# Optimization experiments

Hardware: AMD Instinct MI355X
Metric: run time of the kernel (lower is better)

## Reference

```python
import jax, jax.numpy as jnp
import numpy as np


def setup_inputs() -> dict:
    key = jax.random.key(0)
    kq, kk, kv = jax.random.split(key, 3)
    B, H, S, D = 1, 16, 4096, 64
    Q = jax.random.normal(kq, (B, H, S, D), dtype=jnp.float32)
    K = jax.random.normal(kk, (B, H, S, D), dtype=jnp.float32)
    V = jax.random.normal(kv, (B, H, S, D), dtype=jnp.float32)
    return {"Q": Q, "K": K, "V": V}


def reference(Q, K, V):
    # scores: [B, H, len_q, len_k], scaled by sqrt(dim_k)
    dim_k = K.shape[-1]
    scale = 1.0 / jnp.sqrt(jnp.asarray(dim_k, dtype=Q.dtype))
    scores = jnp.einsum("bhqd,bhkd->bhqk", Q, K) * scale
    attention = jax.nn.softmax(scores, axis=-1)
    context = jnp.einsum("bhqk,bhkd->bhqd", attention, V)
    return context
```

## Files before the change

kernel.cpp:

```cpp
#include <hip/hip_runtime.h>
#include <hip/hip_bf16.h>

typedef short bf16x8 __attribute__((ext_vector_type(8)));
typedef __bf16 bfv8  __attribute__((ext_vector_type(8)));
typedef __bf16 bfv4  __attribute__((ext_vector_type(4)));
typedef float f32x4  __attribute__((ext_vector_type(4)));

#define S_LEN 4096
#define DDIM  64
#define KVB   32
#define QBLK  128
#define NHEAD 16
#define THR   7.0f
#define VOFFB 4096
#define BUFSZ 9216

#define MFMA(a, b, c) __builtin_amdgcn_mfma_f32_16x16x32_bf16((a), (b), (c), 0, 0, 0)

static __device__ __forceinline__ float exp2v(float x) {
    return __builtin_amdgcn_exp2f(x);
}

static __device__ __forceinline__ int4 cvt8(float4 a, float4 b) {
    bfv8 r;
    r[0] = (__bf16)a.x; r[1] = (__bf16)a.y; r[2] = (__bf16)a.z; r[3] = (__bf16)a.w;
    r[4] = (__bf16)b.x; r[5] = (__bf16)b.y; r[6] = (__bf16)b.z; r[7] = (__bf16)b.w;
    return __builtin_bit_cast(int4, r);
}
static __device__ __forceinline__ int2 cvt4(f32x4 a) {
    bfv4 r;
    r[0] = (__bf16)a[0]; r[1] = (__bf16)a[1]; r[2] = (__bf16)a[2]; r[3] = (__bf16)a[3];
    return __builtin_bit_cast(int2, r);
}

static __device__ __forceinline__ bf16x8 ldfrag(const unsigned char* base, int row, int doff) {
    int addr = (row * 128 + doff * 2) ^ ((row & 7) << 4);
    return *reinterpret_cast<const bf16x8*>(base + addr);
}

static __device__ __forceinline__ void stage(unsigned char* base, int kdst, int vdst,
                                             int4 kv, int4 vv) {
    *reinterpret_cast<int4*>(base + kdst)         = kv;
    *reinterpret_cast<int4*>(base + VOFFB + vdst) = vv;
}

static __device__ __forceinline__ bf16x8 softmax_pb(f32x4 s0, f32x4 s1, float& m,
                                                    f32x4 acc[4], f32x4& lacc) {
    float mx = fmaxf(fmaxf(fmaxf(s0[0], s0[1]), s0[2]),
                     fmaxf(fmaxf(s0[3], s1[0]),
                           fmaxf(s1[1], fmaxf(s1[2], s1[3]))));
    if (!__all(mx <= m + THR)) {
        float pm = fmaxf(mx, __shfl_xor(mx, 16));
        pm = fmaxf(pm, __shfl_xor(pm, 32));
        float mn = fmaxf(m, pm);
        float al = exp2v(m - mn);
        #pragma unroll
        for (int dk = 0; dk < 4; ++dk)
            #pragma unroll
            for (int j = 0; j < 4; ++j) acc[dk][j] *= al;
        #pragma unroll
        for (int j = 0; j < 4; ++j) lacc[j] *= al;
        m = mn;
    }
    bfv8 r;
    #pragma unroll
    for (int j = 0; j < 4; ++j) {
        r[2 * j]     = (__bf16)exp2v(s0[j] - m);
        r[2 * j + 1] = (__bf16)exp2v(s1[j] - m);
    }
    return __builtin_bit_cast(bf16x8, r);
}

__global__ __launch_bounds__(256) void prep(
    const float* __restrict__ Kg, const float* __restrict__ Vg,
    unsigned short* __restrict__ wsKT, unsigned short* __restrict__ wsVT)
{
    const int h  = blockIdx.y;
    const int kt = blockIdx.x;
    const int t  = threadIdx.x;
    const int srow = t >> 3;
    const int sd   = (t & 7) * 8;
    const size_t src = (((size_t)h * S_LEN) + (size_t)kt * 32 + srow) * DDIM + sd;

    {
        float4 a = *reinterpret_cast<const float4*>(Kg + src);
        float4 b = *reinterpret_cast<const float4*>(Kg + src + 4);
        const int swK = (srow * 128 + sd * 2) ^ ((srow & 7) << 4);
        *reinterpret_cast<int4*>(reinterpret_cast<char*>(wsKT)
            + ((size_t)(h * 128 + kt) << 12) + swK) = cvt8(a, b);
    }

    __shared__ __align__(16) unsigned short vt[32][68];
    {
        float4 a = *reinterpret_cast<const float4*>(Vg + src);
        float4 b = *reinterpret_cast<const float4*>(Vg + src + 4);
        int4 w = cvt8(a, b);
        int2 lo = {w.x, w.y}, hi = {w.z, w.w};
        *reinterpret_cast<int2*>(&vt[srow][sd])     = lo;
        *reinterpret_cast<int2*>(&vt[srow][sd + 4]) = hi;
    }
    __syncthreads();
    {
        const int d  = t >> 2;
        const int p0 = (t & 3) * 8;
        unsigned short out[8];
        #pragma unroll
        for (int i = 0; i < 8; ++i) {
            int p   = p0 + i;
            int key = 4 * (p >> 3) + ((p & 7) >> 1) + 16 * (p & 1);
            out[i] = vt[key][d];
        }
        *reinterpret_cast<int4*>(wsVT + ((size_t)(h * 128 + kt) * 2048) + d * 32 + p0)
            = *reinterpret_cast<const int4*>(out);
    }
}

template <int KSPLIT>
__global__ __launch_bounds__(256, 4) void attn_fwd(
    const float* __restrict__ Qg, const unsigned short* __restrict__ wsKT,
    const unsigned short* __restrict__ wsVT, float* __restrict__ Og,
    unsigned short* __restrict__ wsO, float* __restrict__ wsML)
{
    const int nwg  = 32 * NHEAD * KSPLIT;
    const int f    = blockIdx.x;
    const int work = (f & 7) * (nwg >> 3) + (f >> 3);
    const int qb   = work & 31;
    const int h    = (work >> 5) & (NHEAD - 1);
    const int ks   = (KSPLIT > 1) ? (work >> 9) : 0;
    const int kt0  = ks * (128 / KSPLIT);
    const int NT   = 128 / KSPLIT;
    const int tid  = threadIdx.x;
    const int lane = tid & 63;
    const int wv   = tid >> 6;
    const int g    = lane >> 4;
    const int r16  = lane & 15;

    __shared__ __align__(16) unsigned char lds[2 * BUFSZ];

    const float QSC = 0.125f * 1.44269504088896f;
    const int qrow0 = qb * QBLK + wv * 32 + r16;
    bf16x8 qf0[2], qf1[2];
    {
        const float* qp0 = Qg + ((size_t)h * S_LEN + qrow0) * DDIM;
        const float* qp1 = qp0 + 16 * DDIM;
        #pragma unroll
        for (int c = 0; c < 2; ++c) {
            float4 x = *reinterpret_cast<const float4*>(qp0 + 32 * c + 8 * g);
            float4 y = *reinterpret_cast<const float4*>(qp0 + 32 * c + 8 * g + 4);
            float4 xs = {x.x * QSC, x.y * QSC, x.z * QSC, x.w * QSC};
            float4 ys = {y.x * QSC, y.y * QSC, y.z * QSC, y.w * QSC};
            qf0[c] = __builtin_bit_cast(bf16x8, cvt8(xs, ys));
            x = *reinterpret_cast<const float4*>(qp1 + 32 * c + 8 * g);
            y = *reinterpret_cast<const float4*>(qp1 + 32 * c + 8 * g + 4);
            xs = {x.x * QSC, x.y * QSC, x.z * QSC, x.w * QSC};
            ys = {y.x * QSC, y.y * QSC, y.z * QSC, y.w * QSC};
            qf1[c] = __builtin_bit_cast(bf16x8, cvt8(xs, ys));
        }
    }

    bf16x8 ones;
    #pragma unroll
    for (int e = 0; e < 8; ++e) ones[e] = (short)0x3F80;

    const int kdst = tid * 16;
    const int vdst = (tid >> 2) * 80 + (tid & 3) * 16;
    const unsigned short* ktp = wsKT + ((size_t)(h * 128 + kt0) * 2048) + tid * 8;
    const unsigned short* vtp = wsVT + ((size_t)(h * 128 + kt0) * 2048)
                              + (tid >> 2) * 32 + (tid & 3) * 8;

    int4 kv = *reinterpret_cast<const int4*>(ktp);
    int4 vv = *reinterpret_cast<const int4*>(vtp);
    stage(lds, kdst, vdst, kv, vv);
    ktp += 2048; vtp += 2048;
    kv = *reinterpret_cast<const int4*>(ktp);
    vv = *reinterpret_cast<const int4*>(vtp);
    __syncthreads();

    const f32x4 z0 = {0.f, 0.f, 0.f, 0.f};
    f32x4 accA[4] = {z0, z0, z0, z0};
    f32x4 accB[4] = {z0, z0, z0, z0};
    f32x4 laccA = z0, laccB = z0;
    float m0 = -INFINITY, m1 = -INFINITY;

    int c = 0;
    for (int kt = 0; kt < NT; ++kt) {
        const unsigned char* Klds = lds + c * BUFSZ;
        const unsigned char* Vlds = Klds + VOFFB;

        if (kt + 1 < NT) {
            stage(lds + (c ^ 1) * BUFSZ, kdst, vdst, kv, vv);
            if (kt + 2 < NT) {
                ktp += 2048; vtp += 2048;
                kv = *reinterpret_cast<const int4*>(ktp);
                vv = *reinterpret_cast<const int4*>(vtp);
            }
        }

        bf16x8 vf[4];
        {
            const unsigned char* vbase = Vlds + r16 * 80 + 16 * g;
            #pragma unroll
            for (int dk = 0; dk < 4; ++dk)
                vf[dk] = *reinterpret_cast<const bf16x8*>(vbase + dk * 1280);
        }

        f32x4 sA0 = z0, sA1 = z0, sB0 = z0, sB1 = z0;
        #pragma unroll
        for (int cc = 0; cc < 2; ++cc) {
            bf16x8 k0 = ldfrag(Klds, r16,      32 * cc + 8 * g);
            bf16x8 k1 = ldfrag(Klds, 16 + r16, 32 * cc + 8 * g);
            sA0 = MFMA(k0, qf0[cc], sA0);
            sA1 = MFMA(k1, qf0[cc], sA1);
            sB0 = MFMA(k0, qf1[cc], sB0);
            sB1 = MFMA(k1, qf1[cc], sB1);
        }

        bf16x8 pbA = softmax_pb(sA0, sA1, m0, accA, laccA);
        bf16x8 pbB = softmax_pb(sB0, sB1, m1, accB, laccB);

        laccA = MFMA(ones, pbA, laccA);
        #pragma unroll
        for (int dk = 0; dk < 4; ++dk) accA[dk] = MFMA(vf[dk], pbA, accA[dk]);
        laccB = MFMA(ones, pbB, laccB);
        #pragma unroll
        for (int dk = 0; dk < 4; ++dk) accB[dk] = MFMA(vf[dk], pbB, accB[dk]);

        __syncthreads();
        c ^= 1;
    }

    if (KSPLIT == 1) {
        float inv0 = 1.0f / laccA[0];
        float* op = Og + ((size_t)h * S_LEN + qrow0) * DDIM;
        #pragma unroll
        for (int dk = 0; dk < 4; ++dk) {
            float4 o = {accA[dk][0] * inv0, accA[dk][1] * inv0,
                        accA[dk][2] * inv0, accA[dk][3] * inv0};
            *reinterpret_cast<float4*>(op + 16 * dk + 4 * g) = o;
        }
        float inv1 = 1.0f / laccB[0];
        op += 16 * DDIM;
        #pragma unroll
        for (int dk = 0; dk < 4; ++dk) {
            float4 o = {accB[dk][0] * inv1, accB[dk][1] * inv1,
                        accB[dk][2] * inv1, accB[dk][3] * inv1};
            *reinterpret_cast<float4*>(op + 16 * dk + 4 * g) = o;
        }
    } else {
        const size_t R0 = (size_t)h * S_LEN + qrow0;
        unsigned short* o0 = wsO + ((size_t)ks * (NHEAD * S_LEN) + R0) * DDIM;
        #pragma unroll
        for (int dk = 0; dk < 4; ++dk)
            *reinterpret_cast<int2*>(o0 + 16 * dk + 4 * g) = cvt4(accA[dk]);
        o0 += 16 * DDIM;
        #pragma unroll
        for (int dk = 0; dk < 4; ++dk)
            *reinterpret_cast<int2*>(o0 + 16 * dk + 4 * g) = cvt4(accB[dk]);
        if (g == 0) {
            float2 v0 = {m0, laccA[0]};
            float2 v1 = {m1, laccB[0]};
            *reinterpret_cast<float2*>(wsML + ((size_t)ks * (NHEAD * S_LEN) + R0) * 2)      = v0;
            *reinterpret_cast<float2*>(wsML + ((size_t)ks * (NHEAD * S_LEN) + R0 + 16) * 2) = v1;
        }
    }
}

template <int NS>
__global__ __launch_bounds__(256) void combineN(
    const unsigned short* __restrict__ wsO, const float* __restrict__ wsML,
    float* __restrict__ Og)
{
    const int NR = NHEAD * S_LEN;
    int t  = blockIdx.x * 256 + threadIdx.x;
    int R  = t >> 4;
    int d4 = (t & 15) * 4;
    float2 ml[NS];
    float m = -INFINITY;
    #pragma unroll
    for (int s = 0; s < NS; ++s) {
        ml[s] = *reinterpret_cast<const float2*>(wsML + ((size_t)s * NR + R) * 2);
        m = fmaxf(m, ml[s].x);
    }
    float a[NS], den = 0.f;
    #pragma unroll
    for (int s = 0; s < NS; ++s) { a[s] = exp2v(ml[s].x - m); den += a[s] * ml[s].y; }
    float inv = 1.0f / den;
    float4 o = {0.f, 0.f, 0.f, 0.f};
    #pragma unroll
    for (int s = 0; s < NS; ++s) {
        bfv4 ob = __builtin_bit_cast(bfv4,
            *reinterpret_cast<const int2*>(wsO + ((size_t)s * NR + R) * DDIM + d4));
        float w = a[s] * inv;
        o.x += w * (float)ob[0]; o.y += w * (float)ob[1];
        o.z += w * (float)ob[2]; o.w += w * (float)ob[3];
    }
    *reinterpret_cast<float4*>(Og + (size_t)R * DDIM + d4) = o;
}

extern "C" void kernel_launch(void* const* d_in, const int* in_sizes, int n_in,
                              void* d_out, int out_size, void* d_ws, size_t ws_size,
                              hipStream_t stream) {
    const float* Q = (const float*)d_in[0];
    const float* K = (const float*)d_in[1];
    const float* V = (const float*)d_in[2];
    float* O = (float*)d_out;

    const size_t nKT = (size_t)NHEAD * 128 * 2048;
    const size_t nVT = (size_t)NHEAD * 128 * 2048;
    const size_t nOrow = (size_t)NHEAD * S_LEN * DDIM;
    const size_t nMLrow = (size_t)NHEAD * S_LEN * 2;
    const size_t baseB  = (nKT + nVT) * 2;
    const size_t perSplitB = nOrow * 2 + nMLrow * 4;
    const size_t need2 = baseB + 2 * perSplitB;

    unsigned short* wsKT = (unsigned short*)d_ws;
    unsigned short* wsVT = wsKT + nKT;
    unsigned short* wsO  = wsVT + nVT;

    prep<<<dim3(128, NHEAD), dim3(256, 1, 1), 0, stream>>>(K, V, wsKT, wsVT);

    if (ws_size >= need2) {
        float* wsML = (float*)(wsO + 2 * nOrow);
        attn_fwd<2><<<dim3(32 * NHEAD * 2), dim3(256, 1, 1), 0, stream>>>(
            Q, wsKT, wsVT, O, wsO, wsML);
        int nthr = NHEAD * S_LEN * (DDIM / 4);
        combineN<2><<<dim3(nthr / 256), dim3(256, 1, 1), 0, stream>>>(wsO, wsML, O);
    } else {
        attn_fwd<1><<<dim3(32 * NHEAD), dim3(256, 1, 1), 0, stream>>>(
            Q, wsKT, wsVT, O, nullptr, nullptr);
    }
}
```

Measured before the change: 102.5 us.

## Software-pipeline PV MFMAs one tile behind QK and softmax in attention loop

Restructures the main KV loop so that the P·V and row-sum MFMAs for the previous tile are issued alongside the QK^T MFMAs of the current tile. V fragments and probabilities are carried across iterations in registers and drained after the loop. The goal is to overlap matrix-core work with the softmax exp/max dependency chain and LDS loads. The extra live registers force launch bounds down from 4 to 3 waves per SIMD, which lowers occupancy.

```diff
diff --git a/kernel.cpp b/kernel.cpp
--- a/kernel.cpp
+++ b/kernel.cpp
@@ -116,7 +116,7 @@
 }
 
 template <int KSPLIT>
-__global__ __launch_bounds__(256, 4) void attn_fwd(
+__global__ __launch_bounds__(256, 3) void attn_fwd(
     const float* __restrict__ Qg, const unsigned short* __restrict__ wsKT,
     const unsigned short* __restrict__ wsVT, float* __restrict__ Og,
     unsigned short* __restrict__ wsO, float* __restrict__ wsML)
@@ -182,10 +182,45 @@
     f32x4 laccA = z0, laccB = z0;
     float m0 = -INFINITY, m1 = -INFINITY;
 
+    const bf16x8 bz = {0, 0, 0, 0, 0, 0, 0, 0};
+    bf16x8 pbAp = bz, pbBp = bz;
+    bf16x8 vfp[4] = {bz, bz, bz, bz};
+
     int c = 0;
     for (int kt = 0; kt < NT; ++kt) {
         const unsigned char* Klds = lds + c * BUFSZ;
         const unsigned char* Vlds = Klds + VOFFB;
+
+        bf16x8 vf[4];
+        {
+            const unsigned char* vbase = Vlds + r16 * 80 + 16 * g;
+            #pragma unroll
+            for (int dk = 0; dk < 4; ++dk)
+                vf[dk] = *reinterpret_cast<const bf16x8*>(vbase + dk * 1280);
+        }
+        bf16x8 k00 = ldfrag(Klds, r16,      8 * g);
+        bf16x8 k10 = ldfrag(Klds, 16 + r16, 8 * g);
+        bf16x8 k01 = ldfrag(Klds, r16,      32 + 8 * g);
+        bf16x8 k11 = ldfrag(Klds, 16 + r16, 32 + 8 * g);
+
+        laccA = MFMA(ones, pbAp, laccA);
+        #pragma unroll
+        for (int dk = 0; dk < 4; ++dk) accA[dk] = MFMA(vfp[dk], pbAp, accA[dk]);
+        laccB = MFMA(ones, pbBp, laccB);
+        #pragma unroll
+        for (int dk = 0; dk < 4; ++dk) accB[dk] = MFMA(vfp[dk], pbBp, accB[dk]);
+
+        f32x4 sA0 = MFMA(k00, qf0[0], z0);
+        f32x4 sA1 = MFMA(k10, qf0[0], z0);
+        f32x4 sB0 = MFMA(k00, qf1[0], z0);
+        f32x4 sB1 = MFMA(k10, qf1[0], z0);
+        sA0 = MFMA(k01, qf0[1], sA0);
+        sA1 = MFMA(k11, qf0[1], sA1);
+        sB0 = MFMA(k01, qf1[1], sB0);
+        sB1 = MFMA(k11, qf1[1], sB1);
+
+        bf16x8 pbA = softmax_pb(sA0, sA1, m0, accA, laccA);
+        bf16x8 pbB = softmax_pb(sB0, sB1, m1, accB, laccB);
 
         if (kt + 1 < NT) {
             stage(lds + (c ^ 1) * BUFSZ, kdst, vdst, kv, vv);
@@ -196,38 +231,20 @@
             }
         }
 
-        bf16x8 vf[4];
-        {
-            const unsigned char* vbase = Vlds + r16 * 80 + 16 * g;
-            #pragma unroll
-            for (int dk = 0; dk < 4; ++dk)
-                vf[dk] = *reinterpret_cast<const bf16x8*>(vbase + dk * 1280);
-        }
-
-        f32x4 sA0 = z0, sA1 = z0, sB0 = z0, sB1 = z0;
-        #pragma unroll
-        for (int cc = 0; cc < 2; ++cc) {
-            bf16x8 k0 = ldfrag(Klds, r16,      32 * cc + 8 * g);
-            bf16x8 k1 = ldfrag(Klds, 16 + r16, 32 * cc + 8 * g);
-            sA0 = MFMA(k0, qf0[cc], sA0);
-            sA1 = MFMA(k1, qf0[cc], sA1);
-            sB0 = MFMA(k0, qf1[cc], sB0);
-            sB1 = MFMA(k1, qf1[cc], sB1);
-        }
-
-        bf16x8 pbA = softmax_pb(sA0, sA1, m0, accA, laccA);
-        bf16x8 pbB = softmax_pb(sB0, sB1, m1, accB, laccB);
-
-        laccA = MFMA(ones, pbA, laccA);
-        #pragma unroll
-        for (int dk = 0; dk < 4; ++dk) accA[dk] = MFMA(vf[dk], pbA, accA[dk]);
-        laccB = MFMA(ones, pbB, laccB);
-        #pragma unroll
-        for (int dk = 0; dk < 4; ++dk) accB[dk] = MFMA(vf[dk], pbB, accB[dk]);
-
         __syncthreads();
+
+        pbAp = pbA; pbBp = pbB;
+        #pragma unroll
+        for (int dk = 0; dk < 4; ++dk) vfp[dk] = vf[dk];
         c ^= 1;
     }
+
+    laccA = MFMA(ones, pbAp, laccA);
+    #pragma unroll
+    for (int dk = 0; dk < 4; ++dk) accA[dk] = MFMA(vfp[dk], pbAp, accA[dk]);
+    laccB = MFMA(ones, pbBp, laccB);
+    #pragma unroll
+    for (int dk = 0; dk < 4; ++dk) accB[dk] = MFMA(vfp[dk], pbBp, accB[dk]);
 
     if (KSPLIT == 1) {
         float inv0 = 1.0f / laccA[0];
```

Result: slower. 105.1 us (+2.5%).
